# Performance work log

Hardware: AMD Instinct MI355X
Metric: run time of the kernel (lower is better)

## Reference

```python
import jax, jax.numpy as jnp
import numpy as np

NH, NP, HD = 8, 4, 32  # num_heads, num_points, head_dim (C=256)


def setup_inputs() -> dict:
    key = jax.random.key(0)
    k = jax.random.split(key, 8)
    B, Nq, H, W, C = 4, 8192, 128, 128, 256
    query = jax.random.normal(k[0], (B, Nq, C), jnp.float32)
    reference_points = jax.random.uniform(k[1], (B, Nq, 2), jnp.float32)
    value = jax.random.normal(k[2], (B, H * W, C), jnp.float32)
    s = 1.0 / np.sqrt(C).astype(np.float32)
    W_off = jax.random.normal(k[3], (C, NH * NP * 2), jnp.float32) * s
    b_off = jax.random.normal(k[4], (NH * NP * 2,), jnp.float32) * 0.5
    W_attn = jax.random.normal(k[5], (C, NH * NP), jnp.float32) * s
    b_attn = jnp.zeros((NH * NP,), jnp.float32)
    W_val = jax.random.normal(k[6], (C, C), jnp.float32) * s
    b_val = jnp.zeros((C,), jnp.float32)
    W_out = jax.random.normal(k[7], (C, C), jnp.float32) * s
    b_out = jnp.zeros((C,), jnp.float32)
    return dict(query=query, reference_points=reference_points, value=value,
                W_off=W_off, b_off=b_off, W_attn=W_attn, b_attn=b_attn,
                W_val=W_val, b_val=b_val, W_out=W_out, b_out=b_out, Hs=H, Ws=W)


def reference(query, reference_points, value, W_off, b_off, W_attn, b_attn,
              W_val, b_val, W_out, b_out, Hs, Ws):
    B, Nq, C = query.shape
    # sampling offsets and attention weights from queries
    off = (query @ W_off + b_off).reshape(B, Nq, NH, NP, 2)
    attn = jax.nn.softmax((query @ W_attn + b_attn).reshape(B, Nq, NH, NP), axis=-1)
    off = jnp.stack([off[..., 0] / Ws * 0.1, off[..., 1] / Hs * 0.1], axis=-1)
    loc = jnp.clip(reference_points[:, :, None, None, :] + off, 0.0, 1.0)  # [B,Nq,NH,NP,2] (x,y)
    # project value and arrange per head: [B, NH, H*W, HD]
    v = (value @ W_val + b_val).reshape(B, Hs, Ws, NH, HD)
    v = v.transpose(0, 3, 1, 2, 4).reshape(B, NH, Hs * Ws, HD)
    # grid_sample bilinear, align_corners=False, padding_mode='border':
    # pixel coord = loc*size - 0.5, clamped to [0, size-1]
    gx = jnp.clip(loc[..., 0] * Ws - 0.5, 0.0, Ws - 1.0)
    gy = jnp.clip(loc[..., 1] * Hs - 0.5, 0.0, Hs - 1.0)
    x0 = jnp.floor(gx); y0 = jnp.floor(gy)
    fx = gx - x0; fy = gy - y0
    x0i = x0.astype(jnp.int32); y0i = y0.astype(jnp.int32)
    x1i = jnp.minimum(x0i + 1, Ws - 1); y1i = jnp.minimum(y0i + 1, Hs - 1)

    def flat(xi, yi):  # [B,Nq,NH,NP] -> [B,NH,Nq*NP]
        return (yi * Ws + xi).transpose(0, 2, 1, 3).reshape(B, NH, Nq * NP)

    def gather(idx):  # -> [B,NH,Nq*NP,HD]
        return jnp.take_along_axis(v, idx[..., None], axis=2)

    def wts(w):  # [B,Nq,NH,NP] -> [B,NH,Nq*NP,1]
        return w.transpose(0, 2, 1, 3).reshape(B, NH, Nq * NP, 1)

    samp = (wts((1 - fx) * (1 - fy)) * gather(flat(x0i, y0i))
            + wts(fx * (1 - fy)) * gather(flat(x1i, y0i))
            + wts((1 - fx) * fy) * gather(flat(x0i, y1i))
            + wts(fx * fy) * gather(flat(x1i, y1i)))
    samp = samp.reshape(B, NH, Nq, NP, HD)
    aw = attn.transpose(0, 2, 1, 3)[..., None]  # [B,NH,Nq,NP,1]
    out = (samp * aw).sum(axis=3)               # [B,NH,Nq,HD]
    out = out.transpose(0, 2, 1, 3).reshape(B, Nq, C)
    return out @ W_out + b_out
```

## Files before the change

kernel.cpp:

```cpp
#include <hip/hip_runtime.h>
#include <cstddef>

#define B_   4
#define NQ_  8192
#define C_   256
#define H_   128
#define W_   128
#define HW_  (H_ * W_)
#define NH_  8
#define NP_  4
#define HD_  32

typedef __attribute__((ext_vector_type(8))) short s16x8;
typedef __attribute__((ext_vector_type(4))) float f32x4;

__device__ __forceinline__ short f2bf(float x) {
    unsigned u = __float_as_uint(x);
    unsigned r = (u + 0x7FFFu + ((u >> 16) & 1u)) >> 16;
    return (short)r;
}
__device__ __forceinline__ unsigned cvt_pk_bf16(float lo, float hi) {
    unsigned r;
    asm("v_cvt_pk_bf16_f32 %0, %1, %2" : "=v"(r) : "v"(lo), "v"(hi));
    return r;
}
__device__ __forceinline__ void gload_lds16(const void* g, void* l) {
    __builtin_amdgcn_global_load_lds(
        (const __attribute__((address_space(1))) void*)g,
        (__attribute__((address_space(3))) void*)l, 16, 0, 0);
}

#define SCHED0 __builtin_amdgcn_sched_barrier(0)
#define VMW2 do { SCHED0; asm volatile("s_waitcnt vmcnt(2)" ::: "memory"); SCHED0; } while (0)
#define VMW0 do { SCHED0; asm volatile("s_waitcnt vmcnt(0)" ::: "memory"); SCHED0; } while (0)
#define LGKM0 do { asm volatile("s_waitcnt lgkmcnt(0)" ::: "memory"); } while (0)

__global__ void prep_kernel(const float* __restrict__ Wv, const float* __restrict__ Wo,
                            const float* __restrict__ Woff, const float* __restrict__ Wattn,
                            const float* __restrict__ boff, const float* __restrict__ battn,
                            short* __restrict__ BtVal, short* __restrict__ BtOut,
                            short* __restrict__ BtOA, float* __restrict__ biasOA)
{
    const int b = blockIdx.x, t = threadIdx.x;
    if (b < 256) {
        const int n = b;
        BtVal[(size_t)n * 256 + t] = f2bf(Wv[(size_t)t * 256 + n]);
    } else if (b < 512) {
        const int n = b - 256;
        BtOut[(size_t)n * 256 + t] = f2bf(Wo[(size_t)t * 256 + n]);
    } else {
        const int n = b - 512;
        float v = (n < 64) ? Woff[(size_t)t * 64 + n]
                           : (n < 96 ? Wattn[(size_t)t * 32 + (n - 64)] : 0.f);
        BtOA[(size_t)n * 256 + t] = f2bf(v);
        if (t == 0) biasOA[n] = (n < 64) ? boff[n] : (n < 96 ? battn[n - 64] : 0.f);
    }
}

__device__ __forceinline__ void stage_B_lds(const short* __restrict__ Bt,
                                            short* Bsm, int tid)
{
    const int w = tid >> 6;
#pragma unroll
    for (int j = 0; j < 16; ++j) {
        const int row = j * 16 + (tid >> 5);
        const int src = (tid & 31) ^ (row & 15);
        gload_lds16(&Bt[(size_t)row * 256 + src * 8],
                    (char*)Bsm + j * 8192 + w * 1024);
    }
}

template<int OM>
__device__ __forceinline__ void do_chunk(
    const float* __restrict__ Af, int m0, const float* __restrict__ bias,
    void* __restrict__ Cp, const short* Bsm, char* As80,
    int tid, int l, int wm, int wn)
{
    const int arow = tid >> 2, aseg = tid & 3;
    const int frag_r = l & 15;
    const int g = l >> 4;

    float4 pend[2][2];
#define ISSUE(kk, slot)                                                       \
    { const float4* p_ = (const float4*)(Af + (size_t)(m0 + arow) * 256       \
                                         + (kk) * 32 + aseg * 8);             \
      pend[slot][0] = p_[0]; pend[slot][1] = p_[1]; }
#define CVTW(slot, buf)                                                       \
    { union { unsigned u[4]; s16x8 v; } pk_;                                  \
      pk_.u[0] = cvt_pk_bf16(pend[slot][0].x, pend[slot][0].y);               \
      pk_.u[1] = cvt_pk_bf16(pend[slot][0].z, pend[slot][0].w);               \
      pk_.u[2] = cvt_pk_bf16(pend[slot][1].x, pend[slot][1].y);               \
      pk_.u[3] = cvt_pk_bf16(pend[slot][1].z, pend[slot][1].w);               \
      *(s16x8*)(As80 + (buf) * 10240 + arow * 80 + aseg * 16) = pk_.v; }

    f32x4 acc[4][4];
#pragma unroll
    for (int i = 0; i < 4; ++i)
#pragma unroll
        for (int j = 0; j < 4; ++j) acc[i][j] = (f32x4)0.f;

    ISSUE(0, 0); ISSUE(1, 1); SCHED0;
    VMW2;
    CVTW(0, 0); LGKM0;
    __builtin_amdgcn_s_barrier();

#pragma unroll
    for (int k = 0; k < 8; ++k) {
        if (k <= 5) { ISSUE(k + 2, k & 1); SCHED0; }
        s16x8 a[4], b[4];
#pragma unroll
        for (int mf = 0; mf < 4; ++mf) {
            const int row = wm * 64 + mf * 16 + frag_r;
            a[mf] = *(const s16x8*)(As80 + (k & 1) * 10240 + row * 80 + g * 16);
        }
#pragma unroll
        for (int nf = 0; nf < 4; ++nf) {
            const int brow = wn * 64 + nf * 16 + frag_r;
            const int phys = (k * 4 + g) ^ (brow & 15);
            b[nf] = *(const s16x8*)((const char*)Bsm + brow * 512 + phys * 16);
        }
#pragma unroll
        for (int mf = 0; mf < 4; ++mf)
#pragma unroll
            for (int nf = 0; nf < 4; ++nf)
                acc[mf][nf] = __builtin_amdgcn_mfma_f32_16x16x32_bf16(
                    a[mf], b[nf], acc[mf][nf], 0, 0, 0);
        if (k < 7) {
            if (k <= 5) { VMW2; } else { VMW0; }
            CVTW((k + 1) & 1, (k + 1) & 1);
            LGKM0;
            __builtin_amdgcn_s_barrier();
        }
    }
#undef ISSUE
#undef CVTW

    const int col_local = wn * 64 + (l & 15);
    const int rbase = wm * 64 + (l >> 4) * 4;
#pragma unroll
    for (int nf = 0; nf < 4; ++nf) {
        const int n = col_local + nf * 16;
        if (OM == 0 && n >= 96) continue;
        const float bs = bias[n];
#pragma unroll
        for (int mf = 0; mf < 4; ++mf) {
            const f32x4 v = acc[mf][nf];
#pragma unroll
            for (int rr = 0; rr < 4; ++rr) {
                const int m = m0 + rbase + mf * 16 + rr;
                const float o = v[rr] + bs;
                if (OM == 0) {
                    ((float*)Cp)[(size_t)m * 128 + n] = o;
                } else {
                    const int bb = m >> 14, pix = m & (HW_ - 1);
                    const int h = n >> 5, d = n & 31;
                    ((short*)Cp)[((size_t)(bb * NH_ + h) * HW_ + pix) * HD_ + d] = f2bf(o);
                }
            }
        }
    }
}

__global__ __launch_bounds__(512, 2)
void pgemm(const float* __restrict__ value, const short* __restrict__ BtVal,
           const float* __restrict__ b_val, short* __restrict__ vproj,
           const float* __restrict__ query, const short* __restrict__ BtOA,
           const float* __restrict__ biasOA, float* __restrict__ oa)
{
    __shared__ __align__(16) short Bsm[256 * 256];
    __shared__ __align__(16) char  As80[2 * 10240];
    const int tid = threadIdx.x;
    const int l = tid & 63;
    const int w = tid >> 6;
    const int wm = w >> 2, wn = w & 3;
    const int bid = blockIdx.x;

    stage_B_lds(BtVal, Bsm, tid);
    do_chunk<2>(value, bid * 256,       b_val, vproj, Bsm, As80, tid, l, wm, wn);
    do_chunk<2>(value, bid * 256 + 128, b_val, vproj, Bsm, As80, tid, l, wm, wn);

    __builtin_amdgcn_s_barrier();
    stage_B_lds(BtOA, Bsm, tid);
    do_chunk<0>(query, bid * 128, biasOA, oa, Bsm, As80, tid, l, wm, wn);
}

__global__ __launch_bounds__(256, 4)
void gemm_k3(const short* __restrict__ A16, const short* __restrict__ Bt,
             const float* __restrict__ bias, float* __restrict__ Cp)
{
    __shared__ char  AsRaw[2 * 8192];
    __shared__ short Bs[2 * 4096];
    const int tid = threadIdx.x;
    const int l = tid & 63;
    const int w = tid >> 6;
    const int wm = w >> 1, wn = w & 1;
    const int m0 = (blockIdx.x >> 1) * 128;
    const int n0 = (blockIdx.x & 1) * 128;

    f32x4 acc[4][4];
#pragma unroll
    for (int i = 0; i < 4; ++i)
#pragma unroll
        for (int j = 0; j < 4; ++j) acc[i][j] = (f32x4)0.f;

    const int frag_r = l & 15;
    const int kslot  = (l >> 4) * 8;

#define STAGE_B3(k0, buf)                                                     \
    _Pragma("unroll")                                                         \
    for (int r = 0; r < 2; ++r) {                                             \
        const int i = r * 256 + tid;                                          \
        gload_lds16(&Bt[(size_t)(n0 + (i >> 2)) * 256 + (k0) + (i & 3) * 8],  \
                    (char*)Bs + (buf) * 8192 + r * 4096 + w * 1024);          \
    }
#define STAGE_A3(k0, buf)                                                     \
    _Pragma("unroll")                                                         \
    for (int r = 0; r < 2; ++r) {                                             \
        const int i = r * 256 + tid;                                          \
        gload_lds16(&A16[(size_t)(m0 + (i >> 2)) * 256 + (k0) + (i & 3) * 8], \
                    AsRaw + (buf) * 8192 + r * 4096 + w * 1024);              \
    }

    STAGE_B3(0, 0);
    STAGE_A3(0, 0);
    __syncthreads();

#pragma unroll
    for (int k = 0; k < 8; ++k) {
        const int cur = k & 1, nxt = cur ^ 1;
        if (k < 7) {
            STAGE_B3((k + 1) * 32, nxt);
            STAGE_A3((k + 1) * 32, nxt);
        }
        s16x8 a[4], b[4];
#pragma unroll
        for (int mf = 0; mf < 4; ++mf)
            a[mf] = *(const s16x8*)(AsRaw + cur * 8192 + (wm * 64 + mf * 16 + frag_r) * 64 + kslot * 2);
#pragma unroll
        for (int nf = 0; nf < 4; ++nf)
            b[nf] = *(const s16x8*)&Bs[cur * 4096 + (wn * 64 + nf * 16 + frag_r) * 32 + kslot];
#pragma unroll
        for (int mf = 0; mf < 4; ++mf)
#pragma unroll
            for (int nf = 0; nf < 4; ++nf)
                acc[mf][nf] = __builtin_amdgcn_mfma_f32_16x16x32_bf16(
                    a[mf], b[nf], acc[mf][nf], 0, 0, 0);
        if (k < 7) __syncthreads();
    }
#undef STAGE_A3
#undef STAGE_B3

    const int col_local = wn * 64 + (l & 15);
    const int rbase = wm * 64 + (l >> 4) * 4;
#pragma unroll
    for (int nf = 0; nf < 4; ++nf) {
        const int n = n0 + col_local + nf * 16;
        const float bs = bias[n];
#pragma unroll
        for (int mf = 0; mf < 4; ++mf) {
            const f32x4 v = acc[mf][nf];
#pragma unroll
            for (int rr = 0; rr < 4; ++rr)
                Cp[(size_t)(m0 + rbase + mf * 16 + rr) * 256 + n] = v[rr] + bs;
        }
    }
}

__global__ __launch_bounds__(256)
void sample_kernel(const float* __restrict__ oa,
                   const float* __restrict__ ref,
                   const short* __restrict__ vproj,
                   short* __restrict__ samp)
{
    __shared__ int4   s_idx[2][32];
    __shared__ float4 s_w[2][32];
    const int tid = threadIdx.x;
    const int q0 = blockIdx.x * 2;

    if (tid < 64) {
        const int qq = tid >> 5;
        const int hp = tid & 31;
        const int h = hp >> 2, p = hp & 3;
        const int q = q0 + qq;
        const float logit = oa[(size_t)q * 128 + 64 + h * 4 + p];
        float mx = fmaxf(logit, __shfl_xor(logit, 1));
        mx = fmaxf(mx, __shfl_xor(mx, 2));
        float e = __expf(logit - mx);
        float s = e + __shfl_xor(e, 1);
        s += __shfl_xor(s, 2);
        const float aw = e / s;

        const float ox = oa[(size_t)q * 128 + h * 8 + p * 2 + 0] * (0.1f / (float)W_);
        const float oy = oa[(size_t)q * 128 + h * 8 + p * 2 + 1] * (0.1f / (float)H_);
        const float lx = fminf(fmaxf(ref[(size_t)q * 2 + 0] + ox, 0.f), 1.f);
        const float ly = fminf(fmaxf(ref[(size_t)q * 2 + 1] + oy, 0.f), 1.f);
        const float gx = fminf(fmaxf(lx * (float)W_ - 0.5f, 0.f), (float)(W_ - 1));
        const float gy = fminf(fmaxf(ly * (float)H_ - 0.5f, 0.f), (float)(H_ - 1));
        const float x0f = floorf(gx), y0f = floorf(gy);
        const float fx = gx - x0f, fy = gy - y0f;
        const int x0 = (int)x0f, y0 = (int)y0f;
        const int x1 = min(x0 + 1, W_ - 1), y1 = min(y0 + 1, H_ - 1);
        s_idx[qq][hp] = make_int4((y0 * W_ + x0) * HD_, (y0 * W_ + x1) * HD_,
                                  (y1 * W_ + x0) * HD_, (y1 * W_ + x1) * HD_);
        const float gx1 = 1.f - fx, gy1 = 1.f - fy;
        s_w[qq][hp] = make_float4(aw * gx1 * gy1, aw * fx * gy1,
                                  aw * gx1 * fy,  aw * fx * fy);
    }
    __syncthreads();

    const int qq = tid >> 7;
    const int t = tid & 127;
    const int h = t >> 4;
    const int d0 = (t & 15) * 2;
    const int q = q0 + qq;
    const int b = q >> 13;
    const short* vh = vproj + (size_t)(b * NH_ + h) * (HW_ * HD_) + d0;

    float a0 = 0.f, a1 = 0.f;
#pragma unroll
    for (int p = 0; p < 4; ++p) {
        const int4   ii = s_idx[qq][h * 4 + p];
        const float4 ww = s_w[qq][h * 4 + p];
        unsigned v;
        v = *(const unsigned*)&vh[ii.x];
        a0 = fmaf(ww.x, __uint_as_float(v << 16), a0);
        a1 = fmaf(ww.x, __uint_as_float(v & 0xFFFF0000u), a1);
        v = *(const unsigned*)&vh[ii.y];
        a0 = fmaf(ww.y, __uint_as_float(v << 16), a0);
        a1 = fmaf(ww.y, __uint_as_float(v & 0xFFFF0000u), a1);
        v = *(const unsigned*)&vh[ii.z];
        a0 = fmaf(ww.z, __uint_as_float(v << 16), a0);
        a1 = fmaf(ww.z, __uint_as_float(v & 0xFFFF0000u), a1);
        v = *(const unsigned*)&vh[ii.w];
        a0 = fmaf(ww.w, __uint_as_float(v << 16), a0);
        a1 = fmaf(ww.w, __uint_as_float(v & 0xFFFF0000u), a1);
    }
    const unsigned lo = (unsigned)(unsigned short)f2bf(a0);
    const unsigned hi = (unsigned)(unsigned short)f2bf(a1);
    ((unsigned*)samp)[((size_t)q * 256 + h * HD_ + d0) >> 1] = lo | (hi << 16);
}

extern "C" void kernel_launch(void* const* d_in, const int* in_sizes, int n_in,
                              void* d_out, int out_size, void* d_ws, size_t ws_size,
                              hipStream_t stream)
{
    const float* query  = (const float*)d_in[0];
    const float* refpt  = (const float*)d_in[1];
    const float* value  = (const float*)d_in[2];
    const float* W_off  = (const float*)d_in[3];
    const float* b_off  = (const float*)d_in[4];
    const float* W_attn = (const float*)d_in[5];
    const float* b_attn = (const float*)d_in[6];
    const float* W_val  = (const float*)d_in[7];
    const float* b_val  = (const float*)d_in[8];
    const float* W_out  = (const float*)d_in[9];
    const float* b_out  = (const float*)d_in[10];
    float* out = (float*)d_out;

    char* ws = (char*)d_ws;
    short* vproj  = (short*)ws;
    short* samp   = (short*)(ws + (size_t)32 * 1024 * 1024);
    float* oa     = (float*)(ws + (size_t)48 * 1024 * 1024);
    short* BtVal  = (short*)(ws + (size_t)64 * 1024 * 1024);
    short* BtOut  = BtVal + 256 * 256;
    short* BtOA   = BtOut + 256 * 256;
    float* biasOA = (float*)(BtOA + 256 * 256);

    prep_kernel<<<768, 256, 0, stream>>>(W_val, W_out, W_off, W_attn,
                                         b_off, b_attn, BtVal, BtOut, BtOA, biasOA);

    pgemm<<<256, 512, 0, stream>>>(value, BtVal, b_val, vproj,
                                   query, BtOA, biasOA, oa);

    sample_kernel<<<(B_ * NQ_) / 2, 256, 0, stream>>>(oa, refpt, vproj, samp);

    gemm_k3<<<512, 256, 0, stream>>>(samp, BtOut, b_out, out);
}
```

Baseline: 76.54 us.

## Load A fragments directly into registers per wave, dropping LDS staging of A

The projection GEMM no longer stages the converted A tile through double-buffered LDS with per-k barriers. Each wave now owns 16 rows and the full 256 output columns. It loads and converts its A fragment straight into MFMA operand registers and sweeps all 16 B fragments from LDS. This removes the A LDS writes and reads and the block barriers inside the k loop, at the cost of reading B from LDS about four times as often per wave and holding a larger accumulator array.

New measurement: 121.6 us. 58.9% more time.

```diff
diff --git a/kernel.cpp b/kernel.cpp
--- a/kernel.cpp
+++ b/kernel.cpp
@@ -29,11 +29,6 @@
         (const __attribute__((address_space(1))) void*)g,
         (__attribute__((address_space(3))) void*)l, 16, 0, 0);
 }
-
-#define SCHED0 __builtin_amdgcn_sched_barrier(0)
-#define VMW2 do { SCHED0; asm volatile("s_waitcnt vmcnt(2)" ::: "memory"); SCHED0; } while (0)
-#define VMW0 do { SCHED0; asm volatile("s_waitcnt vmcnt(0)" ::: "memory"); SCHED0; } while (0)
-#define LGKM0 do { asm volatile("s_waitcnt lgkmcnt(0)" ::: "memory"); } while (0)
 
 __global__ void prep_kernel(const float* __restrict__ Wv, const float* __restrict__ Wo,
                             const float* __restrict__ Woff, const float* __restrict__ Wattn,
@@ -71,91 +66,63 @@
 }
 
 template<int OM>
-__device__ __forceinline__ void do_chunk(
+__device__ __forceinline__ void do_pass(
     const float* __restrict__ Af, int m0, const float* __restrict__ bias,
-    void* __restrict__ Cp, const short* Bsm, char* As80,
-    int tid, int l, int wm, int wn)
-{
-    const int arow = tid >> 2, aseg = tid & 3;
-    const int frag_r = l & 15;
-    const int g = l >> 4;
+    void* __restrict__ Cp, const short* Bsm, int l, int w)
+{
+    const int fr = l & 15;
+    const int g  = l >> 4;
+    const int row = m0 + w * 16 + fr;
+    const float* ap = Af + (size_t)row * 256 + g * 8;
+
+    f32x4 acc[16];
+#pragma unroll
+    for (int nf = 0; nf < 16; ++nf) acc[nf] = (f32x4)0.f;
 
     float4 pend[2][2];
-#define ISSUE(kk, slot)                                                       \
-    { const float4* p_ = (const float4*)(Af + (size_t)(m0 + arow) * 256       \
-                                         + (kk) * 32 + aseg * 8);             \
-      pend[slot][0] = p_[0]; pend[slot][1] = p_[1]; }
-#define CVTW(slot, buf)                                                       \
-    { union { unsigned u[4]; s16x8 v; } pk_;                                  \
-      pk_.u[0] = cvt_pk_bf16(pend[slot][0].x, pend[slot][0].y);               \
-      pk_.u[1] = cvt_pk_bf16(pend[slot][0].z, pend[slot][0].w);               \
-      pk_.u[2] = cvt_pk_bf16(pend[slot][1].x, pend[slot][1].y);               \
-      pk_.u[3] = cvt_pk_bf16(pend[slot][1].z, pend[slot][1].w);               \
-      *(s16x8*)(As80 + (buf) * 10240 + arow * 80 + aseg * 16) = pk_.v; }
-
-    f32x4 acc[4][4];
-#pragma unroll
-    for (int i = 0; i < 4; ++i)
-#pragma unroll
-        for (int j = 0; j < 4; ++j) acc[i][j] = (f32x4)0.f;
-
-    ISSUE(0, 0); ISSUE(1, 1); SCHED0;
-    VMW2;
-    CVTW(0, 0); LGKM0;
-    __builtin_amdgcn_s_barrier();
+    pend[0][0] = *(const float4*)(ap);
+    pend[0][1] = *(const float4*)(ap + 4);
+    pend[1][0] = *(const float4*)(ap + 32);
+    pend[1][1] = *(const float4*)(ap + 36);
 
 #pragma unroll
     for (int k = 0; k < 8; ++k) {
-        if (k <= 5) { ISSUE(k + 2, k & 1); SCHED0; }
-        s16x8 a[4], b[4];
-#pragma unroll
-        for (int mf = 0; mf < 4; ++mf) {
-            const int row = wm * 64 + mf * 16 + frag_r;
-            a[mf] = *(const s16x8*)(As80 + (k & 1) * 10240 + row * 80 + g * 16);
-        }
-#pragma unroll
-        for (int nf = 0; nf < 4; ++nf) {
-            const int brow = wn * 64 + nf * 16 + frag_r;
+        union { unsigned u[4]; s16x8 v; } pk;
+        pk.u[0] = cvt_pk_bf16(pend[k & 1][0].x, pend[k & 1][0].y);
+        pk.u[1] = cvt_pk_bf16(pend[k & 1][0].z, pend[k & 1][0].w);
+        pk.u[2] = cvt_pk_bf16(pend[k & 1][1].x, pend[k & 1][1].y);
+        pk.u[3] = cvt_pk_bf16(pend[k & 1][1].z, pend[k & 1][1].w);
+        const s16x8 a = pk.v;
+        if (k < 6) {
+            pend[k & 1][0] = *(const float4*)(ap + (k + 2) * 32);
+            pend[k & 1][1] = *(const float4*)(ap + (k + 2) * 32 + 4);
+        }
+#pragma unroll
+        for (int nf = 0; nf < 16; ++nf) {
+            const int brow = nf * 16 + fr;
             const int phys = (k * 4 + g) ^ (brow & 15);
-            b[nf] = *(const s16x8*)((const char*)Bsm + brow * 512 + phys * 16);
-        }
-#pragma unroll
-        for (int mf = 0; mf < 4; ++mf)
-#pragma unroll
-            for (int nf = 0; nf < 4; ++nf)
-                acc[mf][nf] = __builtin_amdgcn_mfma_f32_16x16x32_bf16(
-                    a[mf], b[nf], acc[mf][nf], 0, 0, 0);
-        if (k < 7) {
-            if (k <= 5) { VMW2; } else { VMW0; }
-            CVTW((k + 1) & 1, (k + 1) & 1);
-            LGKM0;
-            __builtin_amdgcn_s_barrier();
-        }
-    }
-#undef ISSUE
-#undef CVTW
-
-    const int col_local = wn * 64 + (l & 15);
-    const int rbase = wm * 64 + (l >> 4) * 4;
-#pragma unroll
-    for (int nf = 0; nf < 4; ++nf) {
-        const int n = col_local + nf * 16;
+            const s16x8 b = *(const s16x8*)((const char*)Bsm + brow * 512 + phys * 16);
+            acc[nf] = __builtin_amdgcn_mfma_f32_16x16x32_bf16(a, b, acc[nf], 0, 0, 0);
+        }
+    }
+
+    const int mrow0 = m0 + w * 16 + g * 4;
+#pragma unroll
+    for (int nf = 0; nf < 16; ++nf) {
+        const int n = nf * 16 + fr;
         if (OM == 0 && n >= 96) continue;
         const float bs = bias[n];
-#pragma unroll
-        for (int mf = 0; mf < 4; ++mf) {
-            const f32x4 v = acc[mf][nf];
-#pragma unroll
-            for (int rr = 0; rr < 4; ++rr) {
-                const int m = m0 + rbase + mf * 16 + rr;
-                const float o = v[rr] + bs;
-                if (OM == 0) {
-                    ((float*)Cp)[(size_t)m * 128 + n] = o;
-                } else {
-                    const int bb = m >> 14, pix = m & (HW_ - 1);
-                    const int h = n >> 5, d = n & 31;
-                    ((short*)Cp)[((size_t)(bb * NH_ + h) * HW_ + pix) * HD_ + d] = f2bf(o);
-                }
+        const f32x4 v = acc[nf];
+#pragma unroll
+        for (int rr = 0; rr < 4; ++rr) {
+            const int m = mrow0 + rr;
+            const float o = v[rr] + bs;
+            if (OM == 0) {
+                ((float*)Cp)[(size_t)m * 128 + n] = o;
+            } else {
+                const int bb = m >> 14, pix = m & (HW_ - 1);
+                const int h = n >> 5, d = n & 31;
+                ((short*)Cp)[((size_t)(bb * NH_ + h) * HW_ + pix) * HD_ + d] = f2bf(o);
             }
         }
     }
@@ -168,20 +135,22 @@
            const float* __restrict__ biasOA, float* __restrict__ oa)
 {
     __shared__ __align__(16) short Bsm[256 * 256];
-    __shared__ __align__(16) char  As80[2 * 10240];
     const int tid = threadIdx.x;
     const int l = tid & 63;
     const int w = tid >> 6;
-    const int wm = w >> 2, wn = w & 3;
     const int bid = blockIdx.x;
 
     stage_B_lds(BtVal, Bsm, tid);
-    do_chunk<2>(value, bid * 256,       b_val, vproj, Bsm, As80, tid, l, wm, wn);
-    do_chunk<2>(value, bid * 256 + 128, b_val, vproj, Bsm, As80, tid, l, wm, wn);
-
-    __builtin_amdgcn_s_barrier();
+    __syncthreads();
+
+    do_pass<2>(value, bid * 256,       b_val, vproj, Bsm, l, w);
+    do_pass<2>(value, bid * 256 + 128, b_val, vproj, Bsm, l, w);
+
+    __syncthreads();
     stage_B_lds(BtOA, Bsm, tid);
-    do_chunk<0>(query, bid * 128, biasOA, oa, Bsm, As80, tid, l, wm, wn);
+    __syncthreads();
+
+    do_pass<0>(query, bid * 128, biasOA, oa, Bsm, l, w);
 }
 
 __global__ __launch_bounds__(256, 4)
```

## Split projection GEMM across N halves to double blocks and halve LDS

Applied to the files above, without the earlier changes.

The fused value/query projection kernel now gives each block one 128-column half of the output instead of all 256 columns. This doubles the grid to 512 blocks and halves the staged B tile in LDS, so more blocks can be resident per CU. The A staging buffer drops its 80-byte row padding for a 64-byte stride, and s_setprio brackets the MFMA loops in both GEMMs. In exchange, each fp32 A tile is read and converted twice (once per half), the unpadded stride may cause LDS bank conflicts, and the query projection now runs only in even blocks, which unbalances the work.

Result: slower. 82.66 us (+8.0%).

```diff
diff --git a/kernel.cpp b/kernel.cpp
--- a/kernel.cpp
+++ b/kernel.cpp
@@ -57,24 +57,24 @@
     }
 }
 
-__device__ __forceinline__ void stage_B_lds(const short* __restrict__ Bt,
-                                            short* Bsm, int tid)
+__device__ __forceinline__ void stage_B_half(const short* __restrict__ BtRows,
+                                             short* Bsm, int tid)
 {
     const int w = tid >> 6;
 #pragma unroll
-    for (int j = 0; j < 16; ++j) {
+    for (int j = 0; j < 8; ++j) {
         const int row = j * 16 + (tid >> 5);
         const int src = (tid & 31) ^ (row & 15);
-        gload_lds16(&Bt[(size_t)row * 256 + src * 8],
+        gload_lds16(&BtRows[(size_t)row * 256 + src * 8],
                     (char*)Bsm + j * 8192 + w * 1024);
     }
 }
 
 template<int OM>
-__device__ __forceinline__ void do_chunk(
-    const float* __restrict__ Af, int m0, const float* __restrict__ bias,
-    void* __restrict__ Cp, const short* Bsm, char* As80,
-    int tid, int l, int wm, int wn)
+__device__ __forceinline__ void do_chunk_h(
+    const float* __restrict__ Af, int m0, int nhalf,
+    const float* __restrict__ biasH, void* __restrict__ Cp,
+    const short* Bsm, char* As64, int tid, int l, int wm, int wn)
 {
     const int arow = tid >> 2, aseg = tid & 3;
     const int frag_r = l & 15;
@@ -91,13 +91,13 @@
       pk_.u[1] = cvt_pk_bf16(pend[slot][0].z, pend[slot][0].w);               \
       pk_.u[2] = cvt_pk_bf16(pend[slot][1].x, pend[slot][1].y);               \
       pk_.u[3] = cvt_pk_bf16(pend[slot][1].z, pend[slot][1].w);               \
-      *(s16x8*)(As80 + (buf) * 10240 + arow * 80 + aseg * 16) = pk_.v; }
-
-    f32x4 acc[4][4];
+      *(s16x8*)(As64 + (buf) * 8192 + arow * 64 + aseg * 16) = pk_.v; }
+
+    f32x4 acc[4][2];
 #pragma unroll
     for (int i = 0; i < 4; ++i)
 #pragma unroll
-        for (int j = 0; j < 4; ++j) acc[i][j] = (f32x4)0.f;
+        for (int j = 0; j < 2; ++j) acc[i][j] = (f32x4)0.f;
 
     ISSUE(0, 0); ISSUE(1, 1); SCHED0;
     VMW2;
@@ -107,24 +107,26 @@
 #pragma unroll
     for (int k = 0; k < 8; ++k) {
         if (k <= 5) { ISSUE(k + 2, k & 1); SCHED0; }
-        s16x8 a[4], b[4];
+        s16x8 a[4], b[2];
 #pragma unroll
         for (int mf = 0; mf < 4; ++mf) {
             const int row = wm * 64 + mf * 16 + frag_r;
-            a[mf] = *(const s16x8*)(As80 + (k & 1) * 10240 + row * 80 + g * 16);
-        }
-#pragma unroll
-        for (int nf = 0; nf < 4; ++nf) {
-            const int brow = wn * 64 + nf * 16 + frag_r;
+            a[mf] = *(const s16x8*)(As64 + (k & 1) * 8192 + row * 64 + g * 16);
+        }
+#pragma unroll
+        for (int nf = 0; nf < 2; ++nf) {
+            const int brow = wn * 32 + nf * 16 + frag_r;
             const int phys = (k * 4 + g) ^ (brow & 15);
             b[nf] = *(const s16x8*)((const char*)Bsm + brow * 512 + phys * 16);
         }
+        __builtin_amdgcn_s_setprio(1);
 #pragma unroll
         for (int mf = 0; mf < 4; ++mf)
 #pragma unroll
-            for (int nf = 0; nf < 4; ++nf)
+            for (int nf = 0; nf < 2; ++nf)
                 acc[mf][nf] = __builtin_amdgcn_mfma_f32_16x16x32_bf16(
                     a[mf], b[nf], acc[mf][nf], 0, 0, 0);
+        __builtin_amdgcn_s_setprio(0);
         if (k < 7) {
             if (k <= 5) { VMW2; } else { VMW0; }
             CVTW((k + 1) & 1, (k + 1) & 1);
@@ -135,13 +137,13 @@
 #undef ISSUE
 #undef CVTW
 
-    const int col_local = wn * 64 + (l & 15);
+    const int col_local = wn * 32 + (l & 15);
     const int rbase = wm * 64 + (l >> 4) * 4;
 #pragma unroll
-    for (int nf = 0; nf < 4; ++nf) {
-        const int n = col_local + nf * 16;
-        if (OM == 0 && n >= 96) continue;
-        const float bs = bias[n];
+    for (int nf = 0; nf < 2; ++nf) {
+        const int nloc = col_local + nf * 16;
+        if (OM == 0 && nloc >= 96) continue;
+        const float bs = biasH[nloc];
 #pragma unroll
         for (int mf = 0; mf < 4; ++mf) {
             const f32x4 v = acc[mf][nf];
@@ -150,8 +152,9 @@
                 const int m = m0 + rbase + mf * 16 + rr;
                 const float o = v[rr] + bs;
                 if (OM == 0) {
-                    ((float*)Cp)[(size_t)m * 128 + n] = o;
+                    ((float*)Cp)[(size_t)m * 128 + nloc] = o;
                 } else {
+                    const int n = nhalf * 128 + nloc;
                     const int bb = m >> 14, pix = m & (HW_ - 1);
                     const int h = n >> 5, d = n & 31;
                     ((short*)Cp)[((size_t)(bb * NH_ + h) * HW_ + pix) * HD_ + d] = f2bf(o);
@@ -167,21 +170,28 @@
            const float* __restrict__ query, const short* __restrict__ BtOA,
            const float* __restrict__ biasOA, float* __restrict__ oa)
 {
-    __shared__ __align__(16) short Bsm[256 * 256];
-    __shared__ __align__(16) char  As80[2 * 10240];
+    __shared__ __align__(16) short Bsm[128 * 256];
+    __shared__ __align__(16) char  As64[2 * 8192];
     const int tid = threadIdx.x;
     const int l = tid & 63;
     const int w = tid >> 6;
     const int wm = w >> 2, wn = w & 3;
     const int bid = blockIdx.x;
-
-    stage_B_lds(BtVal, Bsm, tid);
-    do_chunk<2>(value, bid * 256,       b_val, vproj, Bsm, As80, tid, l, wm, wn);
-    do_chunk<2>(value, bid * 256 + 128, b_val, vproj, Bsm, As80, tid, l, wm, wn);
-
-    __builtin_amdgcn_s_barrier();
-    stage_B_lds(BtOA, Bsm, tid);
-    do_chunk<0>(query, bid * 128, biasOA, oa, Bsm, As80, tid, l, wm, wn);
+    const int half = bid & 1;
+    const int mc = bid >> 1;
+
+    stage_B_half(BtVal + (size_t)half * 128 * 256, Bsm, tid);
+
+    do_chunk_h<2>(value, mc * 128, half, b_val + half * 128, vproj,
+                  Bsm, As64, tid, l, wm, wn);
+    do_chunk_h<2>(value, (mc + 256) * 128, half, b_val + half * 128, vproj,
+                  Bsm, As64, tid, l, wm, wn);
+
+    if (half == 0) {
+        __syncthreads();
+        stage_B_half(BtOA, Bsm, tid);
+        do_chunk_h<0>(query, mc * 128, 0, biasOA, oa, Bsm, As64, tid, l, wm, wn);
+    }
 }
 
 __global__ __launch_bounds__(256, 4)
@@ -239,12 +249,14 @@
 #pragma unroll
         for (int nf = 0; nf < 4; ++nf)
             b[nf] = *(const s16x8*)&Bs[cur * 4096 + (wn * 64 + nf * 16 + frag_r) * 32 + kslot];
+        __builtin_amdgcn_s_setprio(1);
 #pragma unroll
         for (int mf = 0; mf < 4; ++mf)
 #pragma unroll
             for (int nf = 0; nf < 4; ++nf)
                 acc[mf][nf] = __builtin_amdgcn_mfma_f32_16x16x32_bf16(
                     a[mf], b[nf], acc[mf][nf], 0, 0, 0);
+        __builtin_amdgcn_s_setprio(0);
         if (k < 7) __syncthreads();
     }
 #undef STAGE_A3
@@ -369,7 +381,7 @@
     prep_kernel<<<768, 256, 0, stream>>>(W_val, W_out, W_off, W_attn,
                                          b_off, b_attn, BtVal, BtOut, BtOA, biasOA);
 
-    pgemm<<<256, 512, 0, stream>>>(value, BtVal, b_val, vproj,
+    pgemm<<<512, 512, 0, stream>>>(value, BtVal, b_val, vproj,
                                    query, BtOA, biasOA, oa);
 
     sample_kernel<<<(B_ * NQ_) / 2, 256, 0, stream>>>(oa, refpt, vproj, samp);
```
